# Optimization experiments

Measured on AMD Instinct MI355X. Metric: run time of the kernel, lower is better.

Reference implementation:

```python
import jax, jax.numpy as jnp
import numpy as np

DIM = 768
HEADS = 12
HEAD_DIM = DIM // HEADS
SCALE = HEAD_DIM ** -0.5


def setup_inputs() -> dict:
    key = jax.random.key(0)
    ks = jax.random.split(key, 6)
    B, N, M, C = 4, 2048, 1024, DIM
    x = jax.random.normal(ks[0], (B, N, C), dtype=jnp.float32)
    r = jax.random.normal(ks[1], (B, M, C), dtype=jnp.float32)
    s = 1.0 / np.sqrt(C)
    W_q = jax.random.normal(ks[2], (C, C), dtype=jnp.float32) * s
    W_kv = jax.random.normal(ks[3], (C, 2 * C), dtype=jnp.float32) * s
    W_proj = jax.random.normal(ks[4], (C, C), dtype=jnp.float32) * s
    b_proj = jax.random.normal(ks[5], (C,), dtype=jnp.float32) * 0.02
    return {"x": x, "r": r, "W_q": W_q, "W_kv": W_kv, "W_proj": W_proj, "b_proj": b_proj}


def reference(x, r, W_q, W_kv, W_proj, b_proj):
    B, N, C = x.shape
    _, M, _ = r.shape
    H, D = HEADS, C // HEADS
    # projections (no bias on q/kv per qkv_bias=False)
    q = (x @ W_q).reshape(B, N, H, D)            # bnhd
    kv = (r @ W_kv).reshape(B, M, 2, H, D)
    k = kv[:, :, 0]                               # bmhd
    v = kv[:, :, 1]                               # bmhd
    attn = jnp.einsum('bnhd,bmhd->bhnm', q, k) * SCALE
    attn = jax.nn.softmax(attn, axis=-1)
    out = jnp.einsum('bhnm,bmhd->bnhd', attn, v).reshape(B, N, C)
    return out @ W_proj + b_proj
```

## Files before the change

### kernel.cpp

```cpp
#include <hip/hip_runtime.h>
#include <hip/hip_bf16.h>
#include <cstdint>

#define HEADS 12

typedef __attribute__((ext_vector_type(8))) __bf16 bf16x8;
typedef __attribute__((ext_vector_type(4))) __bf16 bf16x4;
typedef __attribute__((ext_vector_type(4))) float f32x4;

#define AS1 __attribute__((address_space(1)))
#define AS3 __attribute__((address_space(3)))

__device__ __forceinline__ void gload16(const void* src, void* lds) {
  __builtin_amdgcn_global_load_lds((AS1 void*)src, (AS3 void*)lds, 16, 0, 0);
}

__device__ __forceinline__ uint32_t cvtpk(float lo, float hi) {
  uint32_t r;
  asm("v_cvt_pk_bf16_f32 %0, %1, %2" : "=v"(r) : "v"(lo), "v"(hi));
  return r;
}

__device__ __forceinline__ float exp2_fast(float x) {
  float r;
  asm("v_exp_f32 %0, %1" : "=v"(r) : "v"(x));
  return r;
}

__global__ void k_cast2(const float* __restrict__ x, const float* __restrict__ r,
                        __bf16* __restrict__ xb, __bf16* __restrict__ rb) {
  int i = (blockIdx.x * 256 + threadIdx.x) * 4;
  const float* src;
  __bf16* dst;
  int off;
  if (i < 6291456) { src = x; dst = xb; off = i; }
  else             { src = r; dst = rb; off = i - 6291456; }
  float4 v = *(const float4*)(src + off);
  bf16x4 o;
  o[0] = (__bf16)v.x; o[1] = (__bf16)v.y; o[2] = (__bf16)v.z; o[3] = (__bf16)v.w;
  *(bf16x4*)(dst + off) = o;
}

__global__ void k_twc3(const float* __restrict__ Wq, const float* __restrict__ Wkv,
                       const float* __restrict__ Wp, __bf16* __restrict__ wqt,
                       __bf16* __restrict__ wkvt, __bf16* __restrict__ wpt) {
  __shared__ float tile[32][33];
  const float* W; __bf16* Wt; int N; float scale;
  if (blockIdx.z == 0)      { W = Wq;  Wt = wqt;  N = 768;  scale = 0.18033688011112042f; }
  else if (blockIdx.z == 1) { W = Wkv; Wt = wkvt; N = 1536; scale = 1.0f; }
  else                      { W = Wp;  Wt = wpt;  N = 768;  scale = 1.0f; }
  int nt = blockIdx.x, kt = blockIdx.y;
  if (nt * 32 >= N) return;
  int c = threadIdx.x & 31, r0 = threadIdx.x >> 5;
#pragma unroll
  for (int i = 0; i < 4; ++i) {
    int r = r0 + i * 8;
    tile[r][c] = W[(size_t)(kt * 32 + r) * N + nt * 32 + c];
  }
  __syncthreads();
#pragma unroll
  for (int i = 0; i < 4; ++i) {
    int r = r0 + i * 8;
    Wt[(size_t)(nt * 32 + r) * 768 + kt * 32 + c] = (__bf16)(tile[c][r] * scale);
  }
}

template<bool BF16OUT>
__global__ __launch_bounds__(256, 2) void k_gemm(
    const __bf16* __restrict__ A, const __bf16* __restrict__ Bt,
    void* __restrict__ C, const float* __restrict__ bias, __bf16* __restrict__ vTp,
    int M, int N, int K) {
  __shared__ __align__(16) char ldsA[2][16384];
  __shared__ __align__(16) char ldsB[2][16384];
  const int tid = threadIdx.x;
  const int ln = tid & 63;
  const int w = tid >> 6;
  const int nwx = gridDim.x;
  int bid = blockIdx.y * nwx + blockIdx.x;
  const int cpx = (nwx * gridDim.y) >> 3;
  bid = (bid & 7) * cpx + (bid >> 3);
  const int bm0 = (bid / nwx) * 128, bn0 = (bid % nwx) * 128;
  const int wm0 = (w >> 1) * 64, wn0 = (w & 1) * 64;

  auto stage = [&](char* lds, const __bf16* G, int row0, int k0) {
    const char* gb = (const char*)(G + (size_t)row0 * K + k0);
#pragma unroll
    for (int c = 0; c < 4; ++c) {
      int off = c * 4096 + tid * 16;
      int row = off >> 7;
      int s = ((off >> 4) & 7) ^ (row & 7);
      gload16(gb + (size_t)row * (K * 2) + (s << 4), lds + c * 4096 + (w << 10));
    }
  };

  f32x4 acc[4][4] = {};
  const int NK = K >> 6;
  stage(ldsA[0], A, bm0, 0);
  stage(ldsB[0], Bt, bn0, 0);
  __syncthreads();
  for (int kt = 0; kt < NK; ++kt) {
    const char* bufA = ldsA[kt & 1];
    const char* bufB = ldsB[kt & 1];
    if (kt + 1 < NK) {
      stage(ldsA[(kt + 1) & 1], A, bm0, (kt + 1) << 6);
      stage(ldsB[(kt + 1) & 1], Bt, bn0, (kt + 1) << 6);
    }
    bf16x8 af[2][4], bf[2][4];
#pragma unroll
    for (int kk = 0; kk < 2; ++kk)
#pragma unroll
      for (int mt = 0; mt < 4; ++mt) {
        int row = wm0 + mt * 16 + (ln & 15);
        af[kk][mt] = *(const bf16x8*)(bufA + row * 128 + (((kk * 4 + (ln >> 4)) ^ (row & 7)) << 4));
      }
#pragma unroll
    for (int kk = 0; kk < 2; ++kk)
#pragma unroll
      for (int nt = 0; nt < 4; ++nt) {
        int row = wn0 + nt * 16 + (ln & 15);
        bf[kk][nt] = *(const bf16x8*)(bufB + row * 128 + (((kk * 4 + (ln >> 4)) ^ (row & 7)) << 4));
      }
    __builtin_amdgcn_s_setprio(1);
#pragma unroll
    for (int kk = 0; kk < 2; ++kk)
#pragma unroll
      for (int mt = 0; mt < 4; ++mt)
#pragma unroll
        for (int nt = 0; nt < 4; ++nt)
          acc[mt][nt] = __builtin_amdgcn_mfma_f32_16x16x32_bf16(af[kk][mt], bf[kk][nt], acc[mt][nt], 0, 0, 0);
    __builtin_amdgcn_s_setprio(0);
    __syncthreads();
  }
#pragma unroll
  for (int mt = 0; mt < 4; ++mt) {
    int row = bm0 + wm0 + mt * 16 + ((ln >> 4) << 2);
#pragma unroll
    for (int nt = 0; nt < 4; ++nt) {
      int col = bn0 + wn0 + nt * 16 + (ln & 15);
      if (BF16OUT) {
        if (vTp != nullptr && bn0 >= 768) {
          bf16x4 o;
#pragma unroll
          for (int jj = 0; jj < 4; ++jj) o[jj] = (__bf16)acc[mt][nt][jj];
          *(bf16x4*)(vTp + ((size_t)((row >> 10) * 768 + col - 768)) * 1024 + (row & 1023)) = o;
        } else {
          __bf16* Cb = (__bf16*)C;
#pragma unroll
          for (int jj = 0; jj < 4; ++jj)
            Cb[(size_t)(row + jj) * N + col] = (__bf16)acc[mt][nt][jj];
        }
      } else {
        float* Cf = (float*)C;
        float bv = bias[col];
#pragma unroll
        for (int jj = 0; jj < 4; ++jj)
          Cf[(size_t)(row + jj) * N + col] = acc[mt][nt][jj] + bv;
      }
    }
  }
}

__global__ __launch_bounds__(512, 6) void k_attn(
    const __bf16* __restrict__ q, const __bf16* __restrict__ kv,
    const __bf16* __restrict__ vT, __bf16* __restrict__ ao) {
  __shared__ __align__(16) char ldsK[3][8192];
  __shared__ __align__(16) char ldsV[3][8192];
  const int tid = threadIdx.x, ln = tid & 63, w = tid >> 6, g = ln >> 4;
  const int qt = blockIdx.x, bh = blockIdx.y;
  const int b = bh / HEADS, h = bh % HEADS;
  const int qrow = b * 2048 + qt * 128 + w * 16 + (ln & 15);

  const char* kgb = (const char*)(kv + ((size_t)b * 1024) * 1536 + h * 64);
  const char* vgb = (const char*)(vT + ((size_t)(b * 768 + h * 64)) * 1024);

  const int srow = tid >> 3;
  const int scol = (((tid & 7) ^ (srow & 7)) << 4);
  const int ldst = w * 1024;

  auto stageKV = [&](int t, int buf) {
    gload16(kgb + (size_t)(t * 64 + srow) * 3072 + scol, ldsK[buf] + ldst);
    gload16(vgb + (size_t)srow * 2048 + (size_t)t * 128 + scol, ldsV[buf] + ldst);
  };

  bf16x8 qf[2];
#pragma unroll
  for (int kk = 0; kk < 2; ++kk)
    qf[kk] = *(const bf16x8*)(q + (size_t)qrow * 768 + h * 64 + (kk * 4 + g) * 8);

  stageKV(0, 0);
  stageKV(1, 1);

  f32x4 acc[4] = {};
  float mrow = -1e30f, lrow = 0.f;

  asm volatile("s_waitcnt vmcnt(2)" ::: "memory");
  __builtin_amdgcn_s_barrier();

  for (int t = 0; t < 16; ++t) {
    if (t < 14) stageKV(t + 2, (t + 2) % 3);
    const char* bufK = ldsK[t % 3];
    const char* bufV = ldsV[t % 3];

    f32x4 sf[4] = {};
    __builtin_amdgcn_s_setprio(1);
#pragma unroll
    for (int kk = 0; kk < 2; ++kk)
#pragma unroll
      for (int nt = 0; nt < 4; ++nt) {
        int row = nt * 16 + (ln & 15);
        bf16x8 kf = *(const bf16x8*)(bufK + row * 128 + (((kk * 4 + g) ^ (row & 7)) << 4));
        sf[nt] = __builtin_amdgcn_mfma_f32_16x16x32_bf16(kf, qf[kk], sf[nt], 0, 0, 0);
      }
    __builtin_amdgcn_s_setprio(0);

    float lm = sf[0][0];
#pragma unroll
    for (int nt = 0; nt < 4; ++nt)
#pragma unroll
      for (int jj = 0; jj < 4; ++jj) lm = fmaxf(lm, sf[nt][jj]);
    if (!__all(lm <= mrow + 8.0f)) {
      float mx = lm;
      mx = fmaxf(mx, __shfl_xor(mx, 16, 64));
      mx = fmaxf(mx, __shfl_xor(mx, 32, 64));
      float mn = fmaxf(mrow, mx);
      float corr = exp2_fast(mrow - mn);
      mrow = mn;
      lrow *= corr;
#pragma unroll
      for (int dt = 0; dt < 4; ++dt) acc[dt] *= corr;
    }
    float p[4][4];
    f32x4 ps = {0.f, 0.f, 0.f, 0.f};
#pragma unroll
    for (int nt = 0; nt < 4; ++nt)
#pragma unroll
      for (int jj = 0; jj < 4; ++jj) {
        float e = exp2_fast(sf[nt][jj] - mrow);
        p[nt][jj] = e;
        ps[jj] += e;
      }
    lrow += (ps[0] + ps[1]) + (ps[2] + ps[3]);

    bf16x8 pb[2];
    uint32_t c0[4], c1[4];
#pragma unroll
    for (int nt = 0; nt < 4; ++nt) {
      c0[nt] = cvtpk(p[nt][0], p[nt][1]);
      c1[nt] = cvtpk(p[nt][2], p[nt][3]);
    }
#pragma unroll
    for (int kk = 0; kk < 2; ++kk) {
      uint32_t x0 = c0[2 * kk], y0 = c0[2 * kk + 1];
      asm("v_permlane32_swap_b32 %0, %1" : "+v"(x0), "+v"(y0));
      asm("v_permlane16_swap_b32 %0, %1" : "+v"(x0), "+v"(y0));
      uint32_t x1 = c1[2 * kk], y1 = c1[2 * kk + 1];
      asm("v_permlane32_swap_b32 %0, %1" : "+v"(x1), "+v"(y1));
      asm("v_permlane16_swap_b32 %0, %1" : "+v"(x1), "+v"(y1));
      union { uint32_t u[4]; bf16x8 v; } pk;
      pk.u[0] = x0; pk.u[1] = x1; pk.u[2] = y0; pk.u[3] = y1;
      pb[kk] = pk.v;
    }

    __builtin_amdgcn_s_setprio(1);
#pragma unroll
    for (int kk = 0; kk < 2; ++kk)
#pragma unroll
      for (int dt = 0; dt < 4; ++dt) {
        int row = dt * 16 + (ln & 15);
        bf16x8 vf = *(const bf16x8*)(bufV + row * 128 + (((kk * 4 + g) ^ (row & 7)) << 4));
        acc[dt] = __builtin_amdgcn_mfma_f32_16x16x32_bf16(vf, pb[kk], acc[dt], 0, 0, 0);
      }
    __builtin_amdgcn_s_setprio(0);

    if (t < 14) {
      asm volatile("s_waitcnt vmcnt(2)" ::: "memory");
      __builtin_amdgcn_s_barrier();
    } else if (t == 14) {
      asm volatile("s_waitcnt vmcnt(0)" ::: "memory");
      __builtin_amdgcn_s_barrier();
    }
  }

  float l = lrow;
  l += __shfl_xor(l, 16, 64);
  l += __shfl_xor(l, 32, 64);
  float inv = 1.0f / l;
  size_t rowb = (size_t)qrow * 768 + h * 64;
#pragma unroll
  for (int dt = 0; dt < 4; ++dt) {
    bf16x4 o;
#pragma unroll
    for (int jj = 0; jj < 4; ++jj) o[jj] = (__bf16)(acc[dt][jj] * inv);
    *(bf16x4*)(ao + rowb + 16 * dt + 4 * g) = o;
  }
}

extern "C" void kernel_launch(void* const* d_in, const int* in_sizes, int n_in,
                              void* d_out, int out_size, void* d_ws, size_t ws_size,
                              hipStream_t stream) {
  const float* x = (const float*)d_in[0];
  const float* r = (const float*)d_in[1];
  const float* Wq = (const float*)d_in[2];
  const float* Wkv = (const float*)d_in[3];
  const float* Wp = (const float*)d_in[4];
  const float* bp = (const float*)d_in[5];

  char* ws = (char*)d_ws;
  __bf16* xb  = (__bf16*)ws; ws += (size_t)6291456 * 2;
  __bf16* rb  = (__bf16*)ws; ws += (size_t)3145728 * 2;
  __bf16* wqt = (__bf16*)ws; ws += (size_t)589824 * 2;
  __bf16* wkvt= (__bf16*)ws; ws += (size_t)1179648 * 2;
  __bf16* wpt = (__bf16*)ws; ws += (size_t)589824 * 2;
  __bf16* qb  = (__bf16*)ws; ws += (size_t)6291456 * 2;
  __bf16* kvb = (__bf16*)ws; ws += (size_t)6291456 * 2;
  __bf16* vT  = (__bf16*)ws; ws += (size_t)3145728 * 2;
  __bf16* ao  = (__bf16*)ws;

  k_cast2<<<9216, 256, 0, stream>>>(x, r, xb, rb);
  k_twc3<<<dim3(48, 24, 3), 256, 0, stream>>>(Wq, Wkv, Wp, wqt, wkvt, wpt);
  k_gemm<true><<<dim3(6, 64), 256, 0, stream>>>(xb, wqt, qb, nullptr, nullptr, 8192, 768, 768);
  k_gemm<true><<<dim3(12, 32), 256, 0, stream>>>(rb, wkvt, kvb, nullptr, vT, 4096, 1536, 768);
  k_attn<<<dim3(16, 48), 512, 0, stream>>>(qb, kvb, vT, ao);
  k_gemm<false><<<dim3(6, 64), 256, 0, stream>>>(ao, wpt, d_out, bp, nullptr, 8192, 768, 768);
}
```

Before: 112.2 us.

## Merge Q and KV GEMMs, rewrite attention with 32x32 MFMA and smaller KV tiles

Folds the Q and KV projection GEMMs into one 768-block launch and specializes both GEMMs to fixed shapes. The output-projection GEMM gets its own specialized kernel. Attention now uses 256-thread blocks with 32 query rows per wave and 32x32x16 MFMAs. It iterates 32 KV tiles of 32 keys with a new V swizzle, and block ids are remapped for L2 locality. This aims to cut launch overhead, tail effects and per-MFMA overhead, at the cost of more loop iterations, more barriers and different register pressure.

```diff
diff --git a/kernel.cpp b/kernel.cpp
--- a/kernel.cpp
+++ b/kernel.cpp
@@ -7,6 +7,7 @@
 typedef __attribute__((ext_vector_type(8))) __bf16 bf16x8;
 typedef __attribute__((ext_vector_type(4))) __bf16 bf16x4;
 typedef __attribute__((ext_vector_type(4))) float f32x4;
+typedef __attribute__((ext_vector_type(16))) float f32x16;
 
 #define AS1 __attribute__((address_space(1)))
 #define AS3 __attribute__((address_space(3)))
@@ -65,43 +66,41 @@
   }
 }
 
-template<bool BF16OUT>
-__global__ __launch_bounds__(256, 2) void k_gemm(
-    const __bf16* __restrict__ A, const __bf16* __restrict__ Bt,
-    void* __restrict__ C, const float* __restrict__ bias, __bf16* __restrict__ vTp,
-    int M, int N, int K) {
+__global__ __launch_bounds__(256, 2) void k_gemm12(
+    const __bf16* __restrict__ xb, const __bf16* __restrict__ rb,
+    const __bf16* __restrict__ wqt, const __bf16* __restrict__ wkvt,
+    __bf16* __restrict__ qb, __bf16* __restrict__ kvb, __bf16* __restrict__ vTp) {
   __shared__ __align__(16) char ldsA[2][16384];
   __shared__ __align__(16) char ldsB[2][16384];
   const int tid = threadIdx.x;
   const int ln = tid & 63;
   const int w = tid >> 6;
-  const int nwx = gridDim.x;
-  int bid = blockIdx.y * nwx + blockIdx.x;
-  const int cpx = (nwx * gridDim.y) >> 3;
-  bid = (bid & 7) * cpx + (bid >> 3);
-  const int bm0 = (bid / nwx) * 128, bn0 = (bid % nwx) * 128;
+  int id = blockIdx.x;
+  id = (id & 7) * 96 + (id >> 3);
+  const __bf16* A; const __bf16* Bt; __bf16* C; int N, bm0, bn0; bool qpart;
+  if (id < 384) { A = xb; Bt = wqt;  C = qb;  N = 768;  bm0 = (id / 6) * 128;  bn0 = (id % 6) * 128;  qpart = true; }
+  else { int i2 = id - 384; A = rb; Bt = wkvt; C = kvb; N = 1536; bm0 = (i2 / 12) * 128; bn0 = (i2 % 12) * 128; qpart = false; }
   const int wm0 = (w >> 1) * 64, wn0 = (w & 1) * 64;
 
   auto stage = [&](char* lds, const __bf16* G, int row0, int k0) {
-    const char* gb = (const char*)(G + (size_t)row0 * K + k0);
+    const char* gb = (const char*)(G + (size_t)row0 * 768 + k0);
 #pragma unroll
     for (int c = 0; c < 4; ++c) {
       int off = c * 4096 + tid * 16;
       int row = off >> 7;
       int s = ((off >> 4) & 7) ^ (row & 7);
-      gload16(gb + (size_t)row * (K * 2) + (s << 4), lds + c * 4096 + (w << 10));
+      gload16(gb + (size_t)row * 1536 + (s << 4), lds + c * 4096 + (w << 10));
     }
   };
 
   f32x4 acc[4][4] = {};
-  const int NK = K >> 6;
   stage(ldsA[0], A, bm0, 0);
   stage(ldsB[0], Bt, bn0, 0);
   __syncthreads();
-  for (int kt = 0; kt < NK; ++kt) {
+  for (int kt = 0; kt < 12; ++kt) {
     const char* bufA = ldsA[kt & 1];
     const char* bufB = ldsB[kt & 1];
-    if (kt + 1 < NK) {
+    if (kt + 1 < 12) {
       stage(ldsA[(kt + 1) & 1], A, bm0, (kt + 1) << 6);
       stage(ldsB[(kt + 1) & 1], Bt, bn0, (kt + 1) << 6);
     }
@@ -137,162 +136,223 @@
 #pragma unroll
     for (int nt = 0; nt < 4; ++nt) {
       int col = bn0 + wn0 + nt * 16 + (ln & 15);
-      if (BF16OUT) {
-        if (vTp != nullptr && bn0 >= 768) {
-          bf16x4 o;
-#pragma unroll
-          for (int jj = 0; jj < 4; ++jj) o[jj] = (__bf16)acc[mt][nt][jj];
-          *(bf16x4*)(vTp + ((size_t)((row >> 10) * 768 + col - 768)) * 1024 + (row & 1023)) = o;
-        } else {
-          __bf16* Cb = (__bf16*)C;
-#pragma unroll
-          for (int jj = 0; jj < 4; ++jj)
-            Cb[(size_t)(row + jj) * N + col] = (__bf16)acc[mt][nt][jj];
-        }
+      if (!qpart && bn0 >= 768) {
+        bf16x4 o;
+#pragma unroll
+        for (int jj = 0; jj < 4; ++jj) o[jj] = (__bf16)acc[mt][nt][jj];
+        *(bf16x4*)(vTp + ((size_t)((row >> 10) * 768 + col - 768)) * 1024 + (row & 1023)) = o;
       } else {
-        float* Cf = (float*)C;
-        float bv = bias[col];
 #pragma unroll
         for (int jj = 0; jj < 4; ++jj)
-          Cf[(size_t)(row + jj) * N + col] = acc[mt][nt][jj] + bv;
-      }
-    }
-  }
-}
-
-__global__ __launch_bounds__(512, 6) void k_attn(
+          C[(size_t)(row + jj) * N + col] = (__bf16)acc[mt][nt][jj];
+      }
+    }
+  }
+}
+
+__global__ __launch_bounds__(256, 2) void k_gemmP(
+    const __bf16* __restrict__ A, const __bf16* __restrict__ Bt,
+    float* __restrict__ C, const float* __restrict__ bias) {
+  __shared__ __align__(16) char ldsA[2][16384];
+  __shared__ __align__(16) char ldsB[2][16384];
+  const int tid = threadIdx.x;
+  const int ln = tid & 63;
+  const int w = tid >> 6;
+  int bid = blockIdx.y * 6 + blockIdx.x;
+  bid = (bid & 7) * 48 + (bid >> 3);
+  const int bm0 = (bid / 6) * 128, bn0 = (bid % 6) * 128;
+  const int wm0 = (w >> 1) * 64, wn0 = (w & 1) * 64;
+
+  auto stage = [&](char* lds, const __bf16* G, int row0, int k0) {
+    const char* gb = (const char*)(G + (size_t)row0 * 768 + k0);
+#pragma unroll
+    for (int c = 0; c < 4; ++c) {
+      int off = c * 4096 + tid * 16;
+      int row = off >> 7;
+      int s = ((off >> 4) & 7) ^ (row & 7);
+      gload16(gb + (size_t)row * 1536 + (s << 4), lds + c * 4096 + (w << 10));
+    }
+  };
+
+  f32x4 acc[4][4] = {};
+  stage(ldsA[0], A, bm0, 0);
+  stage(ldsB[0], Bt, bn0, 0);
+  __syncthreads();
+  for (int kt = 0; kt < 12; ++kt) {
+    const char* bufA = ldsA[kt & 1];
+    const char* bufB = ldsB[kt & 1];
+    if (kt + 1 < 12) {
+      stage(ldsA[(kt + 1) & 1], A, bm0, (kt + 1) << 6);
+      stage(ldsB[(kt + 1) & 1], Bt, bn0, (kt + 1) << 6);
+    }
+    bf16x8 af[2][4], bf[2][4];
+#pragma unroll
+    for (int kk = 0; kk < 2; ++kk)
+#pragma unroll
+      for (int mt = 0; mt < 4; ++mt) {
+        int row = wm0 + mt * 16 + (ln & 15);
+        af[kk][mt] = *(const bf16x8*)(bufA + row * 128 + (((kk * 4 + (ln >> 4)) ^ (row & 7)) << 4));
+      }
+#pragma unroll
+    for (int kk = 0; kk < 2; ++kk)
+#pragma unroll
+      for (int nt = 0; nt < 4; ++nt) {
+        int row = wn0 + nt * 16 + (ln & 15);
+        bf[kk][nt] = *(const bf16x8*)(bufB + row * 128 + (((kk * 4 + (ln >> 4)) ^ (row & 7)) << 4));
+      }
+    __builtin_amdgcn_s_setprio(1);
+#pragma unroll
+    for (int kk = 0; kk < 2; ++kk)
+#pragma unroll
+      for (int mt = 0; mt < 4; ++mt)
+#pragma unroll
+        for (int nt = 0; nt < 4; ++nt)
+          acc[mt][nt] = __builtin_amdgcn_mfma_f32_16x16x32_bf16(af[kk][mt], bf[kk][nt], acc[mt][nt], 0, 0, 0);
+    __builtin_amdgcn_s_setprio(0);
+    __syncthreads();
+  }
+#pragma unroll
+  for (int mt = 0; mt < 4; ++mt) {
+    int row = bm0 + wm0 + mt * 16 + ((ln >> 4) << 2);
+#pragma unroll
+    for (int nt = 0; nt < 4; ++nt) {
+      int col = bn0 + wn0 + nt * 16 + (ln & 15);
+      float bv = bias[col];
+#pragma unroll
+      for (int jj = 0; jj < 4; ++jj)
+        C[(size_t)(row + jj) * 768 + col] = acc[mt][nt][jj] + bv;
+    }
+  }
+}
+
+__global__ __launch_bounds__(256, 4) void k_attn(
     const __bf16* __restrict__ q, const __bf16* __restrict__ kv,
     const __bf16* __restrict__ vT, __bf16* __restrict__ ao) {
-  __shared__ __align__(16) char ldsK[3][8192];
-  __shared__ __align__(16) char ldsV[3][8192];
-  const int tid = threadIdx.x, ln = tid & 63, w = tid >> 6, g = ln >> 4;
-  const int qt = blockIdx.x, bh = blockIdx.y;
+  __shared__ __align__(16) char ldsK[3][4096];
+  __shared__ __align__(16) char ldsV[3][4096];
+  const int tid = threadIdx.x, ln = tid & 63, w = tid >> 6;
+  const int l5 = ln >> 5, l32 = ln & 31;
+  int id = blockIdx.y * 16 + blockIdx.x;
+  id = (id & 7) * 96 + (id >> 3);
+  const int qt = id & 15, bh = id >> 4;
   const int b = bh / HEADS, h = bh % HEADS;
-  const int qrow = b * 2048 + qt * 128 + w * 16 + (ln & 15);
+  const int qrow = b * 2048 + qt * 128 + w * 32 + l32;
 
   const char* kgb = (const char*)(kv + ((size_t)b * 1024) * 1536 + h * 64);
   const char* vgb = (const char*)(vT + ((size_t)(b * 768 + h * 64)) * 1024);
 
-  const int srow = tid >> 3;
-  const int scol = (((tid & 7) ^ (srow & 7)) << 4);
-  const int ldst = w * 1024;
+  const int krow = tid >> 3, kc = tid & 7;
+  const size_t ksrc = (size_t)krow * 3072 + (size_t)(((kc ^ (krow & 7)) << 4));
+  const int vrow = tid >> 2, vc = tid & 3;
+  const size_t vsrc = (size_t)vrow * 2048 + (size_t)(((vc ^ ((vrow >> 1) & 3)) << 4));
+  const int ldst = w << 10;
 
   auto stageKV = [&](int t, int buf) {
-    gload16(kgb + (size_t)(t * 64 + srow) * 3072 + scol, ldsK[buf] + ldst);
-    gload16(vgb + (size_t)srow * 2048 + (size_t)t * 128 + scol, ldsV[buf] + ldst);
+    gload16(kgb + (size_t)t * 98304 + ksrc, ldsK[buf] + ldst);
+    gload16(vgb + (size_t)t * 64 + vsrc, ldsV[buf] + ldst);
   };
 
-  bf16x8 qf[2];
-#pragma unroll
-  for (int kk = 0; kk < 2; ++kk)
-    qf[kk] = *(const bf16x8*)(q + (size_t)qrow * 768 + h * 64 + (kk * 4 + g) * 8);
+  bf16x8 qf[4];
+#pragma unroll
+  for (int s = 0; s < 4; ++s)
+    qf[s] = *(const bf16x8*)(q + (size_t)qrow * 768 + h * 64 + 16 * s + 8 * l5);
 
   stageKV(0, 0);
   stageKV(1, 1);
 
-  f32x4 acc[4] = {};
+  f32x16 accO[2] = {};
   float mrow = -1e30f, lrow = 0.f;
 
   asm volatile("s_waitcnt vmcnt(2)" ::: "memory");
   __builtin_amdgcn_s_barrier();
 
-  for (int t = 0; t < 16; ++t) {
-    if (t < 14) stageKV(t + 2, (t + 2) % 3);
+  for (int t = 0; t < 32; ++t) {
+    if (t < 30) stageKV(t + 2, (t + 2) % 3);
     const char* bufK = ldsK[t % 3];
     const char* bufV = ldsV[t % 3];
 
-    f32x4 sf[4] = {};
+    f32x16 s16 = {};
     __builtin_amdgcn_s_setprio(1);
 #pragma unroll
-    for (int kk = 0; kk < 2; ++kk)
-#pragma unroll
-      for (int nt = 0; nt < 4; ++nt) {
-        int row = nt * 16 + (ln & 15);
-        bf16x8 kf = *(const bf16x8*)(bufK + row * 128 + (((kk * 4 + g) ^ (row & 7)) << 4));
-        sf[nt] = __builtin_amdgcn_mfma_f32_16x16x32_bf16(kf, qf[kk], sf[nt], 0, 0, 0);
-      }
+    for (int s = 0; s < 4; ++s) {
+      bf16x8 kf = *(const bf16x8*)(bufK + l32 * 128 + (((2 * s + l5) ^ (l32 & 7)) << 4));
+      s16 = __builtin_amdgcn_mfma_f32_32x32x16_bf16(kf, qf[s], s16, 0, 0, 0);
+    }
     __builtin_amdgcn_s_setprio(0);
 
-    float lm = sf[0][0];
-#pragma unroll
-    for (int nt = 0; nt < 4; ++nt)
-#pragma unroll
-      for (int jj = 0; jj < 4; ++jj) lm = fmaxf(lm, sf[nt][jj]);
+    float lm = s16[0];
+#pragma unroll
+    for (int i = 1; i < 16; ++i) lm = fmaxf(lm, s16[i]);
     if (!__all(lm <= mrow + 8.0f)) {
-      float mx = lm;
-      mx = fmaxf(mx, __shfl_xor(mx, 16, 64));
-      mx = fmaxf(mx, __shfl_xor(mx, 32, 64));
+      float mx = fmaxf(lm, __shfl_xor(lm, 32, 64));
       float mn = fmaxf(mrow, mx);
       float corr = exp2_fast(mrow - mn);
       mrow = mn;
       lrow *= corr;
 #pragma unroll
-      for (int dt = 0; dt < 4; ++dt) acc[dt] *= corr;
-    }
-    float p[4][4];
-    f32x4 ps = {0.f, 0.f, 0.f, 0.f};
-#pragma unroll
-    for (int nt = 0; nt < 4; ++nt)
-#pragma unroll
-      for (int jj = 0; jj < 4; ++jj) {
-        float e = exp2_fast(sf[nt][jj] - mrow);
-        p[nt][jj] = e;
-        ps[jj] += e;
-      }
-    lrow += (ps[0] + ps[1]) + (ps[2] + ps[3]);
-
-    bf16x8 pb[2];
+      for (int dt = 0; dt < 2; ++dt)
+#pragma unroll
+        for (int i = 0; i < 16; ++i) accO[dt][i] *= corr;
+    }
+    float p[16];
+    float ps = 0.f;
+#pragma unroll
+    for (int i = 0; i < 16; ++i) {
+      p[i] = exp2_fast(s16[i] - mrow);
+      ps += p[i];
+    }
+    lrow += ps;
+
     uint32_t c0[4], c1[4];
 #pragma unroll
-    for (int nt = 0; nt < 4; ++nt) {
-      c0[nt] = cvtpk(p[nt][0], p[nt][1]);
-      c1[nt] = cvtpk(p[nt][2], p[nt][3]);
-    }
-#pragma unroll
-    for (int kk = 0; kk < 2; ++kk) {
-      uint32_t x0 = c0[2 * kk], y0 = c0[2 * kk + 1];
-      asm("v_permlane32_swap_b32 %0, %1" : "+v"(x0), "+v"(y0));
-      asm("v_permlane16_swap_b32 %0, %1" : "+v"(x0), "+v"(y0));
-      uint32_t x1 = c1[2 * kk], y1 = c1[2 * kk + 1];
-      asm("v_permlane32_swap_b32 %0, %1" : "+v"(x1), "+v"(y1));
-      asm("v_permlane16_swap_b32 %0, %1" : "+v"(x1), "+v"(y1));
-      union { uint32_t u[4]; bf16x8 v; } pk;
-      pk.u[0] = x0; pk.u[1] = x1; pk.u[2] = y0; pk.u[3] = y1;
-      pb[kk] = pk.v;
-    }
+    for (int j = 0; j < 4; ++j) {
+      c0[j] = cvtpk(p[4 * j], p[4 * j + 1]);
+      c1[j] = cvtpk(p[4 * j + 2], p[4 * j + 3]);
+    }
+    uint32_t w00 = c0[0], w02 = c0[1];
+    asm("v_permlane32_swap_b32 %0, %1" : "+v"(w00), "+v"(w02));
+    uint32_t w01 = c1[0], w03 = c1[1];
+    asm("v_permlane32_swap_b32 %0, %1" : "+v"(w01), "+v"(w03));
+    uint32_t w10 = c0[2], w12 = c0[3];
+    asm("v_permlane32_swap_b32 %0, %1" : "+v"(w10), "+v"(w12));
+    uint32_t w11 = c1[2], w13 = c1[3];
+    asm("v_permlane32_swap_b32 %0, %1" : "+v"(w11), "+v"(w13));
+    union { uint32_t u[4]; bf16x8 v; } pk0, pk1;
+    pk0.u[0] = w00; pk0.u[1] = w01; pk0.u[2] = w02; pk0.u[3] = w03;
+    pk1.u[0] = w10; pk1.u[1] = w11; pk1.u[2] = w12; pk1.u[3] = w13;
 
     __builtin_amdgcn_s_setprio(1);
 #pragma unroll
-    for (int kk = 0; kk < 2; ++kk)
-#pragma unroll
-      for (int dt = 0; dt < 4; ++dt) {
-        int row = dt * 16 + (ln & 15);
-        bf16x8 vf = *(const bf16x8*)(bufV + row * 128 + (((kk * 4 + g) ^ (row & 7)) << 4));
-        acc[dt] = __builtin_amdgcn_mfma_f32_16x16x32_bf16(vf, pb[kk], acc[dt], 0, 0, 0);
-      }
+    for (int dt = 0; dt < 2; ++dt) {
+      int vr = dt * 32 + l32;
+      bf16x8 vf0 = *(const bf16x8*)(bufV + vr * 64 + (((0 + l5) ^ ((vr >> 1) & 3)) << 4));
+      accO[dt] = __builtin_amdgcn_mfma_f32_32x32x16_bf16(vf0, pk0.v, accO[dt], 0, 0, 0);
+      bf16x8 vf1 = *(const bf16x8*)(bufV + vr * 64 + (((2 + l5) ^ ((vr >> 1) & 3)) << 4));
+      accO[dt] = __builtin_amdgcn_mfma_f32_32x32x16_bf16(vf1, pk1.v, accO[dt], 0, 0, 0);
+    }
     __builtin_amdgcn_s_setprio(0);
 
-    if (t < 14) {
+    if (t < 30) {
       asm volatile("s_waitcnt vmcnt(2)" ::: "memory");
       __builtin_amdgcn_s_barrier();
-    } else if (t == 14) {
+    } else if (t == 30) {
       asm volatile("s_waitcnt vmcnt(0)" ::: "memory");
       __builtin_amdgcn_s_barrier();
     }
   }
 
-  float l = lrow;
-  l += __shfl_xor(l, 16, 64);
-  l += __shfl_xor(l, 32, 64);
+  float l = lrow + __shfl_xor(lrow, 32, 64);
   float inv = 1.0f / l;
   size_t rowb = (size_t)qrow * 768 + h * 64;
 #pragma unroll
-  for (int dt = 0; dt < 4; ++dt) {
-    bf16x4 o;
-#pragma unroll
-    for (int jj = 0; jj < 4; ++jj) o[jj] = (__bf16)(acc[dt][jj] * inv);
-    *(bf16x4*)(ao + rowb + 16 * dt + 4 * g) = o;
-  }
+  for (int dt = 0; dt < 2; ++dt)
+#pragma unroll
+    for (int j = 0; j < 4; ++j) {
+      bf16x4 o;
+#pragma unroll
+      for (int i = 0; i < 4; ++i) o[i] = (__bf16)(accO[dt][4 * j + i] * inv);
+      *(bf16x4*)(ao + rowb + dt * 32 + 8 * j + 4 * l5) = o;
+    }
 }
 
 extern "C" void kernel_launch(void* const* d_in, const int* in_sizes, int n_in,
@@ -318,8 +378,7 @@
 
   k_cast2<<<9216, 256, 0, stream>>>(x, r, xb, rb);
   k_twc3<<<dim3(48, 24, 3), 256, 0, stream>>>(Wq, Wkv, Wp, wqt, wkvt, wpt);
-  k_gemm<true><<<dim3(6, 64), 256, 0, stream>>>(xb, wqt, qb, nullptr, nullptr, 8192, 768, 768);
-  k_gemm<true><<<dim3(12, 32), 256, 0, stream>>>(rb, wkvt, kvb, nullptr, vT, 4096, 1536, 768);
-  k_attn<<<dim3(16, 48), 512, 0, stream>>>(qb, kvb, vT, ao);
-  k_gemm<false><<<dim3(6, 64), 256, 0, stream>>>(ao, wpt, d_out, bp, nullptr, 8192, 768, 768);
-}
+  k_gemm12<<<768, 256, 0, stream>>>(xb, rb, wqt, wkvt, qb, kvb, vT);
+  k_attn<<<dim3(16, 48), 256, 0, stream>>>(qb, kvb, vT, ao);
+  k_gemmP<<<dim3(6, 64), 256, 0, stream>>>(ao, wpt, (float*)d_out, bp);
+}
```

Result: faster. 102.4 us (-8.8%).
